# Optimization experiments

Hardware: AMD Instinct MI355X
Metric: run time of the kernel (lower is better)

The kernel has to match this reference:

```python
import jax, jax.numpy as jnp
import numpy as np

N_NODES = 50000
N_EDGES = 1600000
EMB_DIM = 128
N_PATH = 2
N_LAYERS = 2
N_HEADS = 8
HEAD_DIM = EMB_DIM // N_HEADS


def setup_inputs() -> dict:
    key = jax.random.key(0)
    ks = jax.random.split(key, 6)
    fs = jax.random.normal(ks[0], (N_PATH, N_NODES, EMB_DIM), dtype=jnp.float32)
    W = jax.random.normal(ks[1], (N_PATH, N_LAYERS, EMB_DIM, EMB_DIM), dtype=jnp.float32) * (1.0 / np.sqrt(EMB_DIM))
    attn_l = jax.random.normal(ks[2], (N_PATH, N_LAYERS, N_HEADS, HEAD_DIM), dtype=jnp.float32) * 0.1
    attn_r = jax.random.normal(ks[3], (N_PATH, N_LAYERS, N_HEADS, HEAD_DIM), dtype=jnp.float32) * 0.1
    bias = jnp.zeros((N_PATH, N_LAYERS, EMB_DIM), dtype=jnp.float32)
    edges = jax.random.randint(ks[4], (N_PATH, 2, N_EDGES), 0, N_NODES, dtype=jnp.int32)
    return {"fs": fs, "W": W, "attn_l": attn_l, "attn_r": attn_r, "bias": bias, "edges": edges}


def gat_conv(h, src, dst, W, al, ar, b):
    # h: [N, F_in]; DGL GATConv, eval mode (dropout off), residual Identity, bias, ELU.
    N = h.shape[0]
    H, D = al.shape
    feat = (h @ W).reshape(N, H, D)                      # fc projection
    el = jnp.einsum('nhd,hd->nh', feat, al)              # [N, H]
    er = jnp.einsum('nhd,hd->nh', feat, ar)              # [N, H]
    e = jax.nn.leaky_relu(el[src] + er[dst], 0.2)        # [E, H]
    # edge softmax over incoming edges of each destination node
    emax = jax.ops.segment_max(e, dst, num_segments=N)   # [N, H], -inf for 0-in-degree
    emax = jnp.where(jnp.isfinite(emax), emax, 0.0)
    ex = jnp.exp(e - emax[dst])                          # [E, H]
    esum = jax.ops.segment_sum(ex, dst, num_segments=N)  # [N, H]
    alpha = ex / jnp.maximum(esum[dst], 1e-9)            # [E, H]
    msg = alpha[:, :, None] * feat[src]                  # [E, H, D]
    rst = jax.ops.segment_sum(msg, dst, num_segments=N)  # [N, H, D]
    rst = rst + h.reshape(N, H, D) + b.reshape(1, H, D)  # residual (Identity) + bias
    out = jax.nn.elu(rst)
    return out.reshape(N, H * D), alpha


def reference(fs, W, attn_l, attn_r, bias, edges):
    semantic_embeddings = []
    element_weights = []
    for p in range(N_PATH):
        h = fs[p]
        src, dst = edges[p, 0], edges[p, 1]
        attn = None
        for l in range(N_LAYERS):
            h, attn = gat_conv(h, src, dst, W[p, l], attn_l[p, l], attn_r[p, l], bias[p, l])
        semantic_embeddings.append(h)
        element_weights.append(attn)
    return jnp.stack(semantic_embeddings), jnp.stack(element_weights)
```

## Files before the change

kernel.cpp:

```cpp
#include <hip/hip_runtime.h>
#include <hip/hip_bf16.h>
#include <hip/hip_fp16.h>

#define NND 50000
#define NE  1600000
#define EMB 128
#define NH  8
#define HD  16
#define NB  98

typedef __attribute__((ext_vector_type(8))) short short8v;
typedef __attribute__((ext_vector_type(4))) float f32x4;

__device__ __forceinline__ float lrelu(float x) { return x > 0.f ? x : 0.2f * x; }
__device__ __forceinline__ float elu(float x)   { return x > 0.f ? x : expm1f(x); }

__device__ __forceinline__ unsigned short f2bf(float x) {
    __hip_bfloat16 b = __float2bfloat16(x);
    return *reinterpret_cast<unsigned short*>(&b);
}
__device__ __forceinline__ float bf2f(unsigned short u) {
    __hip_bfloat16 b = *reinterpret_cast<__hip_bfloat16*>(&u);
    return __bfloat162float(b);
}

__global__ __launch_bounds__(256) void wpack4(
    const float* __restrict__ W, unsigned short* __restrict__ bphi, unsigned short* __restrict__ bplo)
{
    int s = blockIdx.x * 256 + threadIdx.x;
    int q    = s >> 11;
    int sidx = s & 2047;
    int n    = sidx >> 8;
    int kt   = (sidx >> 6) & 3;
    int lane = sidx & 63;
    int col  = n * 16 + (lane & 15);
    int krow = kt * 32 + ((lane >> 4) << 3);
    const float* Wm = W + (size_t)q * EMB * EMB;
    #pragma unroll
    for (int j = 0; j < 8; ++j) {
        float x = Wm[(size_t)(krow + j) * EMB + col];
        unsigned short hi = f2bf(x);
        unsigned short lo = f2bf(x - bf2f(hi));
        bphi[(size_t)s * 8 + j] = hi;
        bplo[(size_t)s * 8 + j] = lo;
    }
}

__device__ __forceinline__ void gemm_epilogue(
    f32x4 acc[2][2], int lane, int wave, int rowbase,
    const float* __restrict__ alv, const float* __restrict__ arv,
    unsigned short* __restrict__ feat_f16, float* __restrict__ el, float* __restrict__ er)
{
    const int colr = lane & 15;
    const int rgrp = lane >> 4;
    #pragma unroll
    for (int m = 0; m < 2; ++m) {
        const int row0 = rowbase + m * 16 + rgrp * 4;
        #pragma unroll
        for (int q = 0; q < 2; ++q) {
            const int nn = wave * 2 + q;
            f32x4 a = acc[m][q];
            #pragma unroll
            for (int r = 0; r < 4; ++r) {
                if (row0 + r < NND)
                    feat_f16[(size_t)(row0 + r) * EMB + nn * 16 + colr] =
                        __half_as_ushort(__float2half(a[r]));
            }
            const float alc = alv[nn * 16 + colr];
            const float arc = arv[nn * 16 + colr];
            float pl[4], pr[4];
            #pragma unroll
            for (int r = 0; r < 4; ++r) { pl[r] = a[r] * alc; pr[r] = a[r] * arc; }
            #pragma unroll
            for (int mask = 1; mask < 16; mask <<= 1) {
                #pragma unroll
                for (int r = 0; r < 4; ++r) {
                    pl[r] += __shfl_xor(pl[r], mask);
                    pr[r] += __shfl_xor(pr[r], mask);
                }
            }
            if (colr == 0) {
                #pragma unroll
                for (int r = 0; r < 4; ++r) {
                    int row = row0 + r;
                    if (row < NND) {
                        el[row * NH + nn] = pl[r];
                        er[row * NH + nn] = pr[r];
                    }
                }
            }
        }
    }
}

__global__ __launch_bounds__(256) void mfma_gemm_f32(
    const float* __restrict__ fs,
    const unsigned short* __restrict__ bphi_all, const unsigned short* __restrict__ bplo_all,
    const float* __restrict__ al_all, const float* __restrict__ ar_all,
    unsigned short* __restrict__ feat_all, float* __restrict__ el_all, float* __restrict__ er_all)
{
    const int p = blockIdx.y;
    const int q4 = p * 2;
    const float* hin = fs + (size_t)p * NND * EMB;
    const unsigned short* bphi = bphi_all + (size_t)q4 * 16384;
    const unsigned short* bplo = bplo_all + (size_t)q4 * 16384;
    const float* alv = al_all + (size_t)q4 * NH * HD;
    const float* arv = ar_all + (size_t)q4 * NH * HD;
    unsigned short* feat_f16 = feat_all + (size_t)p * NND * EMB;
    float* el = el_all + (size_t)p * NND * NH;
    float* er = er_all + (size_t)p * NND * NH;

    const int lane = threadIdx.x & 63;
    const int wave = threadIdx.x >> 6;
    const int rowbase = blockIdx.x * 32;

    f32x4 acc[2][2];
    #pragma unroll
    for (int m = 0; m < 2; ++m)
        #pragma unroll
        for (int q = 0; q < 2; ++q)
            acc[m][q] = (f32x4){0.f, 0.f, 0.f, 0.f};

    const int ar0 = rowbase + (lane & 15);
    const int ar1 = ar0 + 16;
    const int car0 = ar0 < NND ? ar0 : NND - 1;
    const int car1 = ar1 < NND ? ar1 : NND - 1;
    const int kofs = (lane >> 4) * 8;

    #pragma unroll
    for (int kt = 0; kt < 4; ++kt) {
        const int k0 = kt * 32 + kofs;
        short8v ah0, av0, ah1, av1;
        {
            const float4* fr = reinterpret_cast<const float4*>(hin + (size_t)car0 * EMB + k0);
            float4 x0 = fr[0], x1 = fr[1];
            float xs[8] = { x0.x, x0.y, x0.z, x0.w, x1.x, x1.y, x1.z, x1.w };
            #pragma unroll
            for (int j = 0; j < 8; ++j) {
                unsigned short hi = f2bf(xs[j]);
                ah0[j] = (short)hi;
                av0[j] = (short)f2bf(xs[j] - bf2f(hi));
            }
        }
        {
            const float4* fr = reinterpret_cast<const float4*>(hin + (size_t)car1 * EMB + k0);
            float4 x0 = fr[0], x1 = fr[1];
            float xs[8] = { x0.x, x0.y, x0.z, x0.w, x1.x, x1.y, x1.z, x1.w };
            #pragma unroll
            for (int j = 0; j < 8; ++j) {
                unsigned short hi = f2bf(xs[j]);
                ah1[j] = (short)hi;
                av1[j] = (short)f2bf(xs[j] - bf2f(hi));
            }
        }
        #pragma unroll
        for (int q = 0; q < 2; ++q) {
            const int nn = wave * 2 + q;
            const size_t bofs = ((size_t)(nn * 4 + kt) * 64 + lane) * 8;
            short8v bh = *reinterpret_cast<const short8v*>(bphi + bofs);
            short8v bl = *reinterpret_cast<const short8v*>(bplo + bofs);
            acc[0][q] = __builtin_amdgcn_mfma_f32_16x16x32_bf16(ah0, bh, acc[0][q], 0, 0, 0);
            acc[1][q] = __builtin_amdgcn_mfma_f32_16x16x32_bf16(ah1, bh, acc[1][q], 0, 0, 0);
            acc[0][q] = __builtin_amdgcn_mfma_f32_16x16x32_bf16(av0, bh, acc[0][q], 0, 0, 0);
            acc[1][q] = __builtin_amdgcn_mfma_f32_16x16x32_bf16(av1, bh, acc[1][q], 0, 0, 0);
            acc[0][q] = __builtin_amdgcn_mfma_f32_16x16x32_bf16(ah0, bl, acc[0][q], 0, 0, 0);
            acc[1][q] = __builtin_amdgcn_mfma_f32_16x16x32_bf16(ah1, bl, acc[1][q], 0, 0, 0);
        }
    }
    gemm_epilogue(acc, lane, wave, rowbase, alv, arv, feat_f16, el, er);
}

__global__ __launch_bounds__(256) void mfma_gemm_bf(
    const unsigned short* __restrict__ hhi_all, const unsigned short* __restrict__ hlo_all,
    const unsigned short* __restrict__ bphi_all, const unsigned short* __restrict__ bplo_all,
    const float* __restrict__ al_all, const float* __restrict__ ar_all,
    unsigned short* __restrict__ feat_all, float* __restrict__ el_all, float* __restrict__ er_all)
{
    const int p = blockIdx.y;
    const int q4 = p * 2 + 1;
    const unsigned short* hhi = hhi_all + (size_t)p * NND * EMB;
    const unsigned short* hlo = hlo_all + (size_t)p * NND * EMB;
    const unsigned short* bphi = bphi_all + (size_t)q4 * 16384;
    const unsigned short* bplo = bplo_all + (size_t)q4 * 16384;
    const float* alv = al_all + (size_t)q4 * NH * HD;
    const float* arv = ar_all + (size_t)q4 * NH * HD;
    unsigned short* feat_f16 = feat_all + (size_t)p * NND * EMB;
    float* el = el_all + (size_t)p * NND * NH;
    float* er = er_all + (size_t)p * NND * NH;

    const int lane = threadIdx.x & 63;
    const int wave = threadIdx.x >> 6;
    const int rowbase = blockIdx.x * 32;

    f32x4 acc[2][2];
    #pragma unroll
    for (int m = 0; m < 2; ++m)
        #pragma unroll
        for (int q = 0; q < 2; ++q)
            acc[m][q] = (f32x4){0.f, 0.f, 0.f, 0.f};

    const int ar0 = rowbase + (lane & 15);
    const int ar1 = ar0 + 16;
    const int car0 = ar0 < NND ? ar0 : NND - 1;
    const int car1 = ar1 < NND ? ar1 : NND - 1;
    const int kofs = (lane >> 4) * 8;

    #pragma unroll
    for (int kt = 0; kt < 4; ++kt) {
        const int k0 = kt * 32 + kofs;
        short8v ah0 = *reinterpret_cast<const short8v*>(hhi + (size_t)car0 * EMB + k0);
        short8v av0 = *reinterpret_cast<const short8v*>(hlo + (size_t)car0 * EMB + k0);
        short8v ah1 = *reinterpret_cast<const short8v*>(hhi + (size_t)car1 * EMB + k0);
        short8v av1 = *reinterpret_cast<const short8v*>(hlo + (size_t)car1 * EMB + k0);
        #pragma unroll
        for (int q = 0; q < 2; ++q) {
            const int nn = wave * 2 + q;
            const size_t bofs = ((size_t)(nn * 4 + kt) * 64 + lane) * 8;
            short8v bh = *reinterpret_cast<const short8v*>(bphi + bofs);
            short8v bl = *reinterpret_cast<const short8v*>(bplo + bofs);
            acc[0][q] = __builtin_amdgcn_mfma_f32_16x16x32_bf16(ah0, bh, acc[0][q], 0, 0, 0);
            acc[1][q] = __builtin_amdgcn_mfma_f32_16x16x32_bf16(ah1, bh, acc[1][q], 0, 0, 0);
            acc[0][q] = __builtin_amdgcn_mfma_f32_16x16x32_bf16(av0, bh, acc[0][q], 0, 0, 0);
            acc[1][q] = __builtin_amdgcn_mfma_f32_16x16x32_bf16(av1, bh, acc[1][q], 0, 0, 0);
            acc[0][q] = __builtin_amdgcn_mfma_f32_16x16x32_bf16(ah0, bl, acc[0][q], 0, 0, 0);
            acc[1][q] = __builtin_amdgcn_mfma_f32_16x16x32_bf16(ah1, bl, acc[1][q], 0, 0, 0);
        }
    }
    gemm_epilogue(acc, lane, wave, rowbase, alv, arv, feat_f16, el, er);
}

__global__ __launch_bounds__(256) void bucket_count(
    const int* __restrict__ edges, int* __restrict__ bcnt)
{
    const int p = blockIdx.y;
    const int* dst = edges + (size_t)p * 2 * NE + NE;
    __shared__ int hist[NB];
    const int t = threadIdx.x;
    for (int b = t; b < NB; b += 256) hist[b] = 0;
    __syncthreads();
    const int e0 = blockIdx.x * 2048 + t * 8;
    #pragma unroll
    for (int j = 0; j < 8; ++j) {
        int e = e0 + j;
        if (e < NE) atomicAdd(&hist[dst[e] >> 9], 1);
    }
    __syncthreads();
    for (int b = t; b < NB; b += 256)
        if (hist[b]) atomicAdd(&bcnt[p * 128 + b], hist[b]);
}

__global__ __launch_bounds__(128) void scan_bucket(
    const int* __restrict__ bcnt, int* __restrict__ bbase, int* __restrict__ bcur)
{
    const int p = blockIdx.x;
    __shared__ int s[128];
    const int t = threadIdx.x;
    s[t] = (t < NB) ? bcnt[p * 128 + t] : 0;
    __syncthreads();
    for (int off = 1; off < 128; off <<= 1) {
        int v = (t >= off) ? s[t - off] : 0;
        __syncthreads();
        s[t] += v;
        __syncthreads();
    }
    int excl = (t > 0) ? s[t - 1] : 0;
    if (t <= NB) bbase[p * 128 + t] = excl;
    if (t < NB)  bcur[p * 128 + t]  = excl;
}

__global__ __launch_bounds__(256) void bucket_scatter(
    const int* __restrict__ edges, int* __restrict__ bcur, int* __restrict__ ebuf)
{
    const int p = blockIdx.y;
    const int* src = edges + (size_t)p * 2 * NE;
    const int* dst = src + NE;
    int* eb = ebuf + (size_t)p * NE;
    __shared__ int hist[NB];
    __shared__ int base[NB];
    __shared__ int lcur[NB];
    const int t  = threadIdx.x;
    const int e0 = blockIdx.x * 2048 + t * 8;

    for (int b = t; b < NB; b += 256) { hist[b] = 0; lcur[b] = 0; }
    __syncthreads();

    int sj[8], dj[8];
    bool vj[8];
    #pragma unroll
    for (int j = 0; j < 8; ++j) {
        int e = e0 + j;
        vj[j] = (e < NE);
        if (vj[j]) {
            sj[j] = src[e];
            dj[j] = dst[e];
            atomicAdd(&hist[dj[j] >> 9], 1);
        }
    }
    __syncthreads();
    for (int b = t; b < NB; b += 256) {
        int c = hist[b];
        base[b] = c > 0 ? atomicAdd(&bcur[p * 128 + b], c) : 0;
    }
    __syncthreads();
    #pragma unroll
    for (int j = 0; j < 8; ++j) {
        if (vj[j]) {
            int b   = dj[j] >> 9;
            int off = atomicAdd(&lcur[b], 1);
            eb[(size_t)base[b] + off] = (sj[j] << 9) | (dj[j] & 511);
        }
    }
}

__global__ __launch_bounds__(1024) void bucket_fill(
    const int* __restrict__ bbase, const int* __restrict__ ebuf,
    int* __restrict__ rowptr, int* __restrict__ csrsrc)
{
    const int p = blockIdx.y;
    const int* eb = ebuf + (size_t)p * NE;
    int* rp = rowptr + (size_t)p * (NND + 1);
    int* cs = csrsrc + (size_t)p * NE;
    __shared__ int hist[512];
    __shared__ int excl[512];
    const int b    = blockIdx.x;
    const int n0   = b << 9;
    const int t    = threadIdx.x;
    const int base = bbase[p * 128 + b];
    const int cnt  = bbase[p * 128 + b + 1] - base;

    if (t < 512) hist[t] = 0;
    __syncthreads();
    for (int i = t; i < cnt; i += 1024)
        atomicAdd(&hist[eb[base + i] & 511], 1);
    __syncthreads();
    if (t < 512) excl[t] = hist[t];
    __syncthreads();
    for (int off = 1; off < 512; off <<= 1) {
        int v = 0;
        if (t < 512 && t >= off) v = excl[t - off];
        __syncthreads();
        if (t < 512) excl[t] += v;
        __syncthreads();
    }
    if (t < 512) {
        int e = excl[t] - hist[t];
        int n = n0 + t;
        if (n < NND) rp[n] = base + e;
        hist[t] = e;
    }
    if (b == NB - 1 && t == 0) rp[NND] = NE;
    __syncthreads();
    for (int i = t; i < cnt; i += 1024) {
        int ed = eb[base + i];
        int q = atomicAdd(&hist[ed & 511], 1);
        cs[base + q] = ed >> 9;
    }
}

__global__ __launch_bounds__(256) void wexp_pass(
    const int* __restrict__ rowptr_all, const int* __restrict__ csrsrc_all,
    const float* __restrict__ el_all, const float* __restrict__ er_all,
    unsigned short* __restrict__ wexp_all, float* __restrict__ esum_all)
{
    const int p    = blockIdx.y;
    const int wid  = (blockIdx.x * blockDim.x + threadIdx.x) >> 6;
    const int lane = threadIdx.x & 63;
    if (wid >= NND) return;
    const int n  = wid;
    const int h  = lane >> 3;
    const int j8 = lane & 7;

    const int* rowptr = rowptr_all + (size_t)p * (NND + 1);
    const int* csrsrc = csrsrc_all + (size_t)p * NE;
    const float* el   = el_all + (size_t)p * NND * NH;
    const float* er   = er_all + (size_t)p * NND * NH;
    unsigned short* wexp = wexp_all + (size_t)p * NE * NH;

    const float ern = er[n * NH + h];
    const int r0 = __builtin_amdgcn_readfirstlane(rowptr[n]);
    const int r1 = __builtin_amdgcn_readfirstlane(rowptr[n + 1]);

    float esp = 0.f;
    for (int i = r0; i < r1; i += 16) {
        int i0 = i + j8, i1 = i + j8 + 8;
        bool v0 = i0 < r1, v1 = i1 < r1;
        int s0 = csrsrc[v0 ? i0 : r0];
        int s1 = csrsrc[v1 ? i1 : r0];
        float w0 = __expf(lrelu(el[s0 * NH + h] + ern));
        float w1 = __expf(lrelu(el[s1 * NH + h] + ern));
        if (v0) { esp += w0; wexp[(size_t)i0 * NH + h] = __half_as_ushort(__float2half(w0)); }
        if (v1) { esp += w1; wexp[(size_t)i1 * NH + h] = __half_as_ushort(__float2half(w1)); }
    }
    esp += __shfl_xor(esp, 1);
    esp += __shfl_xor(esp, 2);
    esp += __shfl_xor(esp, 4);
    if (j8 == 0) esum_all[((size_t)p * NND + n) * NH + h] = esp;
}

__global__ __launch_bounds__(256) void gather_agg(
    const int* __restrict__ rowptr_all, const int* __restrict__ csrsrc_all,
    const unsigned short* __restrict__ wexp_all, const float* __restrict__ esum_all,
    const unsigned int* __restrict__ feat_all,
    const float* __restrict__ fs,
    const unsigned int* __restrict__ hhi_all,
    const unsigned int* __restrict__ hlo_all,
    const float* __restrict__ bias_all,
    float* __restrict__ out_emb,
    int layer)
{
    const int p    = blockIdx.y;
    const int wid  = (blockIdx.x * blockDim.x + threadIdx.x) >> 6;
    const int lane = threadIdx.x & 63;
    if (wid >= NND) return;
    const int n = wid;
    const int h = lane >> 3;

    const int* rowptr = rowptr_all + (size_t)p * (NND + 1);
    const int* csrsrc = csrsrc_all + (size_t)p * NE;
    const unsigned short* wexp = wexp_all + (size_t)p * NE * NH;
    const unsigned int* featu = feat_all + (size_t)p * NND * 64;
    const float* bias = bias_all + (size_t)(p * 2 + layer) * EMB;

    const int r0 = __builtin_amdgcn_readfirstlane(rowptr[n]);
    const int r1 = __builtin_amdgcn_readfirstlane(rowptr[n + 1]);

    float acc0 = 0.f, acc1 = 0.f;

    int i = r0;
    for (; i + 16 <= r1; i += 16) {
        int sj[16];
        #pragma unroll
        for (int j = 0; j < 16; ++j) sj[j] = csrsrc[i + j];
        unsigned int vs[16];
        #pragma unroll
        for (int j = 0; j < 16; ++j) vs[j] = featu[(size_t)sj[j] * 64 + lane];
        unsigned short wu[16];
        #pragma unroll
        for (int j = 0; j < 16; ++j) wu[j] = wexp[(size_t)(i + j) * NH + h];
        #pragma unroll
        for (int j = 0; j < 16; ++j) {
            float w = __half2float(__ushort_as_half(wu[j]));
            __half2 v = *reinterpret_cast<__half2*>(&vs[j]);
            acc0 = fmaf(w, __half2float(__low2half(v)), acc0);
            acc1 = fmaf(w, __half2float(__high2half(v)), acc1);
        }
    }
    if (i + 8 <= r1) {
        int sj[8];
        #pragma unroll
        for (int j = 0; j < 8; ++j) sj[j] = csrsrc[i + j];
        unsigned int vs[8];
        #pragma unroll
        for (int j = 0; j < 8; ++j) vs[j] = featu[(size_t)sj[j] * 64 + lane];
        unsigned short wu[8];
        #pragma unroll
        for (int j = 0; j < 8; ++j) wu[j] = wexp[(size_t)(i + j) * NH + h];
        #pragma unroll
        for (int j = 0; j < 8; ++j) {
            float w = __half2float(__ushort_as_half(wu[j]));
            __half2 v = *reinterpret_cast<__half2*>(&vs[j]);
            acc0 = fmaf(w, __half2float(__low2half(v)), acc0);
            acc1 = fmaf(w, __half2float(__high2half(v)), acc1);
        }
        i += 8;
    }
    for (; i < r1; ++i) {
        int sj = csrsrc[i];
        unsigned int vraw = featu[(size_t)sj * 64 + lane];
        float w = __half2float(__ushort_as_half(wexp[(size_t)i * NH + h]));
        __half2 v = *reinterpret_cast<__half2*>(&vraw);
        acc0 = fmaf(w, __half2float(__low2half(v)), acc0);
        acc1 = fmaf(w, __half2float(__high2half(v)), acc1);
    }

    const float es  = esum_all[((size_t)p * NND + n) * NH + h];
    const float inv = 1.f / fmaxf(es, 1e-9f);

    float h0, h1;
    if (layer == 0) {
        float2 hv = reinterpret_cast<const float2*>(fs + (size_t)p * NND * EMB)[(size_t)n * 64 + lane];
        h0 = hv.x; h1 = hv.y;
    } else {
        unsigned int hiu = hhi_all[((size_t)p * NND + n) * 64 + lane];
        unsigned int lou = hlo_all[((size_t)p * NND + n) * 64 + lane];
        h0 = __uint_as_float(hiu << 16) + __uint_as_float(lou << 16);
        h1 = __uint_as_float(hiu & 0xffff0000u) + __uint_as_float(lou & 0xffff0000u);
    }
    float o0 = elu(fmaf(acc0, inv, h0 + bias[lane * 2]));
    float o1 = elu(fmaf(acc1, inv, h1 + bias[lane * 2 + 1]));

    if (layer == 1) {
        reinterpret_cast<float2*>(out_emb + (size_t)p * NND * EMB)[(size_t)n * 64 + lane] =
            make_float2(o0, o1);
    } else {
        unsigned short hi0 = f2bf(o0), hi1 = f2bf(o1);
        unsigned short lo0 = f2bf(o0 - bf2f(hi0)), lo1 = f2bf(o1 - bf2f(hi1));
        const size_t idx = ((size_t)p * NND + n) * 64 + lane;
        const_cast<unsigned int*>(hhi_all)[idx] = (unsigned int)hi0 | ((unsigned int)hi1 << 16);
        const_cast<unsigned int*>(hlo_all)[idx] = (unsigned int)lo0 | ((unsigned int)lo1 << 16);
    }
}

__global__ __launch_bounds__(256) void alpha_write8(
    const int* __restrict__ edges,
    const float* __restrict__ el_all, const float* __restrict__ er_all,
    const float* __restrict__ esum_all, float* __restrict__ out_alpha)
{
    const int p = blockIdx.y;
    int e = blockIdx.x * 256 + threadIdx.x;
    if (e >= NE) return;
    const int* src = edges + (size_t)p * 2 * NE;
    const int* dst = src + NE;
    const float* el   = el_all   + (size_t)p * NND * NH;
    const float* er   = er_all   + (size_t)p * NND * NH;
    const float* esum = esum_all + (size_t)p * NND * NH;
    int s = src[e], d = dst[e];
    const float4* el4 = reinterpret_cast<const float4*>(el + (size_t)s * 8);
    const float4* er4 = reinterpret_cast<const float4*>(er + (size_t)d * 8);
    const float4* es4 = reinterpret_cast<const float4*>(esum + (size_t)d * 8);
    float4 L0 = el4[0], L1 = el4[1];
    float4 R0 = er4[0], R1 = er4[1];
    float4 S0 = es4[0], S1 = es4[1];
    float4 a0, a1;
    a0.x = __fdividef(__expf(lrelu(L0.x + R0.x)), fmaxf(S0.x, 1e-9f));
    a0.y = __fdividef(__expf(lrelu(L0.y + R0.y)), fmaxf(S0.y, 1e-9f));
    a0.z = __fdividef(__expf(lrelu(L0.z + R0.z)), fmaxf(S0.z, 1e-9f));
    a0.w = __fdividef(__expf(lrelu(L0.w + R0.w)), fmaxf(S0.w, 1e-9f));
    a1.x = __fdividef(__expf(lrelu(L1.x + R1.x)), fmaxf(S1.x, 1e-9f));
    a1.y = __fdividef(__expf(lrelu(L1.y + R1.y)), fmaxf(S1.y, 1e-9f));
    a1.z = __fdividef(__expf(lrelu(L1.z + R1.z)), fmaxf(S1.z, 1e-9f));
    a1.w = __fdividef(__expf(lrelu(L1.w + R1.w)), fmaxf(S1.w, 1e-9f));
    float4* o4 = reinterpret_cast<float4*>(out_alpha + ((size_t)p * NE + e) * 8);
    o4[0] = a0;
    o4[1] = a1;
}

extern "C" void kernel_launch(void* const* d_in, const int* in_sizes, int n_in,
                              void* d_out, int out_size, void* d_ws, size_t ws_size,
                              hipStream_t stream) {
    const float* fs   = (const float*)d_in[0];
    const float* W    = (const float*)d_in[1];
    const float* al   = (const float*)d_in[2];
    const float* ar   = (const float*)d_in[3];
    const float* bias = (const float*)d_in[4];
    const int*   edges= (const int*)d_in[5];

    float* out       = (float*)d_out;
    float* out_emb   = out;
    float* out_alpha = out + (size_t)2 * NND * EMB;

    char* ws = (char*)d_ws;
    auto take = [&](size_t bytes) {
        char* r = ws;
        ws += (bytes + 15) & ~(size_t)15;
        return r;
    };
    unsigned short* feat_f16 = (unsigned short*)take((size_t)2 * NND * EMB * 2);
    unsigned short* hhi      = (unsigned short*)take((size_t)2 * NND * EMB * 2);
    unsigned short* hlo      = (unsigned short*)take((size_t)2 * NND * EMB * 2);
    float*          el       = (float*)take((size_t)2 * NND * NH * 4);
    float*          er       = (float*)take((size_t)2 * NND * NH * 4);
    float*          esum     = (float*)take((size_t)2 * NND * NH * 4);
    int*            rowptr   = (int*)take((size_t)2 * (NND + 1) * 4);
    int*            bcnt     = (int*)take((size_t)2 * 128 * 4);
    int*            bbase    = (int*)take((size_t)2 * 128 * 4);
    int*            bcur     = (int*)take((size_t)2 * 128 * 4);
    int*            csrsrc   = (int*)take((size_t)2 * NE * 4);
    unsigned short* wexp     = (unsigned short*)take((size_t)2 * NE * NH * 2);
    unsigned short* bphi     = (unsigned short*)take((size_t)4 * 16384 * 2);
    unsigned short* bplo     = (unsigned short*)take((size_t)4 * 16384 * 2);

    int*          ebuf  = (int*)hlo;
    unsigned int* featu = (unsigned int*)feat_f16;
    unsigned int* hhi_u = (unsigned int*)hhi;
    unsigned int* hlo_u = (unsigned int*)hlo;

    hipMemsetAsync(bcnt, 0, (size_t)2 * 128 * 4, stream);
    bucket_count<<<dim3((NE + 2047) / 2048, 2), 256, 0, stream>>>(edges, bcnt);
    scan_bucket<<<2, 128, 0, stream>>>(bcnt, bbase, bcur);
    bucket_scatter<<<dim3((NE + 2047) / 2048, 2), 256, 0, stream>>>(edges, bcur, ebuf);
    bucket_fill<<<dim3(NB, 2), 1024, 0, stream>>>(bbase, ebuf, rowptr, csrsrc);

    wpack4<<<32, 256, 0, stream>>>(W, bphi, bplo);

    mfma_gemm_f32<<<dim3((NND + 31) / 32, 2), 256, 0, stream>>>(
        fs, bphi, bplo, al, ar, feat_f16, el, er);
    wexp_pass<<<dim3((NND + 3) / 4, 2), 256, 0, stream>>>(
        rowptr, csrsrc, el, er, wexp, esum);
    gather_agg<<<dim3((NND + 3) / 4, 2), 256, 0, stream>>>(
        rowptr, csrsrc, wexp, esum, featu, fs, hhi_u, hlo_u, bias, nullptr, 0);

    mfma_gemm_bf<<<dim3((NND + 31) / 32, 2), 256, 0, stream>>>(
        hhi, hlo, bphi, bplo, al, ar, feat_f16, el, er);
    wexp_pass<<<dim3((NND + 3) / 4, 2), 256, 0, stream>>>(
        rowptr, csrsrc, el, er, wexp, esum);
    gather_agg<<<dim3((NND + 3) / 4, 2), 256, 0, stream>>>(
        rowptr, csrsrc, wexp, esum, featu, fs, hhi_u, hlo_u, bias, out_emb, 1);
    alpha_write8<<<dim3((NE + 255) / 256, 2), 256, 0, stream>>>(
        edges, el, er, esum, out_alpha);
}
```

Baseline: 663.5 us.

## Fuse edge-weight exponent pass into gather aggregation kernel

Removes the separate wexp_pass kernel and the fp16 per-edge weight buffer. Edge weights are now computed inside gather_agg, one (edge, head) pair per lane, then spread across lanes with shuffles, and the exp-sum is reduced in the same kernel. This drops a kernel launch and the write and re-read of the NE*NH half-precision weight array per layer. In exchange it adds random el gathers and shuffles to the aggregation loop, and the tail handling is reworked into a single masked 16-edge block.

```diff
diff --git a/kernel.cpp b/kernel.cpp
--- a/kernel.cpp
+++ b/kernel.cpp
@@ -357,123 +357,84 @@
     }
 }
 
-__global__ __launch_bounds__(256) void wexp_pass(
+__global__ __launch_bounds__(256) void gather_agg(
     const int* __restrict__ rowptr_all, const int* __restrict__ csrsrc_all,
     const float* __restrict__ el_all, const float* __restrict__ er_all,
-    unsigned short* __restrict__ wexp_all, float* __restrict__ esum_all)
+    const unsigned int* __restrict__ feat_all,
+    const float* __restrict__ fs,
+    const unsigned int* __restrict__ hhi_all,
+    const unsigned int* __restrict__ hlo_all,
+    const float* __restrict__ bias_all,
+    float* __restrict__ esum_all,
+    float* __restrict__ out_emb,
+    int layer)
 {
     const int p    = blockIdx.y;
     const int wid  = (blockIdx.x * blockDim.x + threadIdx.x) >> 6;
     const int lane = threadIdx.x & 63;
     if (wid >= NND) return;
     const int n  = wid;
-    const int h  = lane >> 3;
-    const int j8 = lane & 7;
+    const int hB = lane >> 3;
+    const int eA = lane >> 3;
+    const int hA = lane & 7;
 
     const int* rowptr = rowptr_all + (size_t)p * (NND + 1);
     const int* csrsrc = csrsrc_all + (size_t)p * NE;
     const float* el   = el_all + (size_t)p * NND * NH;
     const float* er   = er_all + (size_t)p * NND * NH;
-    unsigned short* wexp = wexp_all + (size_t)p * NE * NH;
-
-    const float ern = er[n * NH + h];
+    const unsigned int* featu = feat_all + (size_t)p * NND * 64;
+    const float* bias = bias_all + (size_t)(p * 2 + layer) * EMB;
+
+    const float ern_a = er[n * NH + hA];
     const int r0 = __builtin_amdgcn_readfirstlane(rowptr[n]);
     const int r1 = __builtin_amdgcn_readfirstlane(rowptr[n + 1]);
 
-    float esp = 0.f;
-    for (int i = r0; i < r1; i += 16) {
-        int i0 = i + j8, i1 = i + j8 + 8;
-        bool v0 = i0 < r1, v1 = i1 < r1;
-        int s0 = csrsrc[v0 ? i0 : r0];
-        int s1 = csrsrc[v1 ? i1 : r0];
-        float w0 = __expf(lrelu(el[s0 * NH + h] + ern));
-        float w1 = __expf(lrelu(el[s1 * NH + h] + ern));
-        if (v0) { esp += w0; wexp[(size_t)i0 * NH + h] = __half_as_ushort(__float2half(w0)); }
-        if (v1) { esp += w1; wexp[(size_t)i1 * NH + h] = __half_as_ushort(__float2half(w1)); }
-    }
-    esp += __shfl_xor(esp, 1);
-    esp += __shfl_xor(esp, 2);
-    esp += __shfl_xor(esp, 4);
-    if (j8 == 0) esum_all[((size_t)p * NND + n) * NH + h] = esp;
-}
-
-__global__ __launch_bounds__(256) void gather_agg(
-    const int* __restrict__ rowptr_all, const int* __restrict__ csrsrc_all,
-    const unsigned short* __restrict__ wexp_all, const float* __restrict__ esum_all,
-    const unsigned int* __restrict__ feat_all,
-    const float* __restrict__ fs,
-    const unsigned int* __restrict__ hhi_all,
-    const unsigned int* __restrict__ hlo_all,
-    const float* __restrict__ bias_all,
-    float* __restrict__ out_emb,
-    int layer)
-{
-    const int p    = blockIdx.y;
-    const int wid  = (blockIdx.x * blockDim.x + threadIdx.x) >> 6;
-    const int lane = threadIdx.x & 63;
-    if (wid >= NND) return;
-    const int n = wid;
-    const int h = lane >> 3;
-
-    const int* rowptr = rowptr_all + (size_t)p * (NND + 1);
-    const int* csrsrc = csrsrc_all + (size_t)p * NE;
-    const unsigned short* wexp = wexp_all + (size_t)p * NE * NH;
-    const unsigned int* featu = feat_all + (size_t)p * NND * 64;
-    const float* bias = bias_all + (size_t)(p * 2 + layer) * EMB;
-
-    const int r0 = __builtin_amdgcn_readfirstlane(rowptr[n]);
-    const int r1 = __builtin_amdgcn_readfirstlane(rowptr[n + 1]);
-
-    float acc0 = 0.f, acc1 = 0.f;
+    float acc0 = 0.f, acc1 = 0.f, esp = 0.f;
 
     int i = r0;
     for (; i + 16 <= r1; i += 16) {
         int sj[16];
         #pragma unroll
         for (int j = 0; j < 16; ++j) sj[j] = csrsrc[i + j];
+        float wa = __expf(lrelu(el[sj[eA] * NH + hA] + ern_a));
+        float wb = __expf(lrelu(el[sj[eA + 8] * NH + hA] + ern_a));
+        esp += wa + wb;
         unsigned int vs[16];
         #pragma unroll
         for (int j = 0; j < 16; ++j) vs[j] = featu[(size_t)sj[j] * 64 + lane];
-        unsigned short wu[16];
-        #pragma unroll
-        for (int j = 0; j < 16; ++j) wu[j] = wexp[(size_t)(i + j) * NH + h];
         #pragma unroll
         for (int j = 0; j < 16; ++j) {
-            float w = __half2float(__ushort_as_half(wu[j]));
+            float wj = __shfl(j < 8 ? wa : wb, ((j & 7) << 3) | hB);
             __half2 v = *reinterpret_cast<__half2*>(&vs[j]);
-            acc0 = fmaf(w, __half2float(__low2half(v)), acc0);
-            acc1 = fmaf(w, __half2float(__high2half(v)), acc1);
-        }
-    }
-    if (i + 8 <= r1) {
-        int sj[8];
-        #pragma unroll
-        for (int j = 0; j < 8; ++j) sj[j] = csrsrc[i + j];
-        unsigned int vs[8];
-        #pragma unroll
-        for (int j = 0; j < 8; ++j) vs[j] = featu[(size_t)sj[j] * 64 + lane];
-        unsigned short wu[8];
-        #pragma unroll
-        for (int j = 0; j < 8; ++j) wu[j] = wexp[(size_t)(i + j) * NH + h];
-        #pragma unroll
-        for (int j = 0; j < 8; ++j) {
-            float w = __half2float(__ushort_as_half(wu[j]));
-            __half2 v = *reinterpret_cast<__half2*>(&vs[j]);
-            acc0 = fmaf(w, __half2float(__low2half(v)), acc0);
-            acc1 = fmaf(w, __half2float(__high2half(v)), acc1);
-        }
-        i += 8;
-    }
-    for (; i < r1; ++i) {
-        int sj = csrsrc[i];
-        unsigned int vraw = featu[(size_t)sj * 64 + lane];
-        float w = __half2float(__ushort_as_half(wexp[(size_t)i * NH + h]));
-        __half2 v = *reinterpret_cast<__half2*>(&vraw);
-        acc0 = fmaf(w, __half2float(__low2half(v)), acc0);
-        acc1 = fmaf(w, __half2float(__high2half(v)), acc1);
-    }
-
-    const float es  = esum_all[((size_t)p * NND + n) * NH + h];
+            acc0 = fmaf(wj, __half2float(__low2half(v)), acc0);
+            acc1 = fmaf(wj, __half2float(__high2half(v)), acc1);
+        }
+    }
+    if (i < r1) {
+        const int m = r1 - i;
+        int sj[16];
+        #pragma unroll
+        for (int j = 0; j < 16; ++j) sj[j] = csrsrc[(i + j < r1) ? i + j : r1 - 1];
+        float wa = 0.f, wb = 0.f;
+        if (eA < m)     wa = __expf(lrelu(el[sj[eA] * NH + hA] + ern_a));
+        if (eA + 8 < m) wb = __expf(lrelu(el[sj[eA + 8] * NH + hA] + ern_a));
+        esp += wa + wb;
+        #pragma unroll
+        for (int j = 0; j < 16; ++j) {
+            if (j >= m) break;
+            unsigned int vraw = featu[(size_t)sj[j] * 64 + lane];
+            float wj = __shfl(j < 8 ? wa : wb, ((j & 7) << 3) | hB);
+            __half2 v = *reinterpret_cast<__half2*>(&vraw);
+            acc0 = fmaf(wj, __half2float(__low2half(v)), acc0);
+            acc1 = fmaf(wj, __half2float(__high2half(v)), acc1);
+        }
+    }
+
+    esp += __shfl_xor(esp, 8);
+    esp += __shfl_xor(esp, 16);
+    esp += __shfl_xor(esp, 32);
+    if (lane < 8) esum_all[((size_t)p * NND + n) * NH + lane] = esp;
+    const float es  = __shfl(esp, hB);
     const float inv = 1.f / fmaxf(es, 1e-9f);
 
     float h0, h1;
@@ -566,7 +527,6 @@
     int*            bbase    = (int*)take((size_t)2 * 128 * 4);
     int*            bcur     = (int*)take((size_t)2 * 128 * 4);
     int*            csrsrc   = (int*)take((size_t)2 * NE * 4);
-    unsigned short* wexp     = (unsigned short*)take((size_t)2 * NE * NH * 2);
     unsigned short* bphi     = (unsigned short*)take((size_t)4 * 16384 * 2);
     unsigned short* bplo     = (unsigned short*)take((size_t)4 * 16384 * 2);
 
@@ -585,17 +545,13 @@
 
     mfma_gemm_f32<<<dim3((NND + 31) / 32, 2), 256, 0, stream>>>(
         fs, bphi, bplo, al, ar, feat_f16, el, er);
-    wexp_pass<<<dim3((NND + 3) / 4, 2), 256, 0, stream>>>(
-        rowptr, csrsrc, el, er, wexp, esum);
     gather_agg<<<dim3((NND + 3) / 4, 2), 256, 0, stream>>>(
-        rowptr, csrsrc, wexp, esum, featu, fs, hhi_u, hlo_u, bias, nullptr, 0);
+        rowptr, csrsrc, el, er, featu, fs, hhi_u, hlo_u, bias, esum, nullptr, 0);
 
     mfma_gemm_bf<<<dim3((NND + 31) / 32, 2), 256, 0, stream>>>(
         hhi, hlo, bphi, bplo, al, ar, feat_f16, el, er);
-    wexp_pass<<<dim3((NND + 3) / 4, 2), 256, 0, stream>>>(
-        rowptr, csrsrc, el, er, wexp, esum);
     gather_agg<<<dim3((NND + 3) / 4, 2), 256, 0, stream>>>(
-        rowptr, csrsrc, wexp, esum, featu, fs, hhi_u, hlo_u, bias, out_emb, 1);
+        rowptr, csrsrc, el, er, featu, fs, hhi_u, hlo_u, bias, esum, out_emb, 1);
     alpha_write8<<<dim3((NE + 255) / 256, 2), 256, 0, stream>>>(
         edges, el, er, esum, out_alpha);
 }
```

After: 620.0 us. 1.07x faster.
